# Optimization experiments

Measured on AMD Instinct MI355X. Metric: run time of the kernel, lower is better.

Reference implementation:

```python
import jax, jax.numpy as jnp
import numpy as np

B, S, H = 2, 1024, 4096
NH, NKV, HD = 32, 8, 128
GROUPS = NH // NKV  # 4


def _dequant_linear(x, w_q, scale, bias=None):
    # torch Linear layout: W [out, in]; per-output-channel symmetric dequant
    w = w_q.astype(jnp.float32) * scale[:, None]
    y = jnp.einsum('bsi,oi->bso', x, w)
    if bias is not None:
        y = y + bias
    return y


def setup_inputs() -> dict:
    key = jax.random.key(0)
    ks = jax.random.split(key, 12)
    hidden_states = jax.random.normal(ks[0], (B, S, H), dtype=jnp.float32)
    # additive causal mask: 0 on/below diagonal, large negative above
    causal = jnp.where(jnp.tril(jnp.ones((S, S), dtype=bool)), 0.0, -1e9).astype(jnp.float32)
    attention_mask = jnp.broadcast_to(causal[None, None], (B, 1, S, S))
    # int8-valued quantized weights, per-out-channel scales (~unit-variance effective weight rows / sqrt(fan_in))
    def qw(k, out, inp):
        return jax.random.randint(k, (out, inp), -127, 128, dtype=jnp.int32)
    def sc(k, out):
        return jax.random.uniform(k, (out,), dtype=jnp.float32, minval=1e-4, maxval=3e-4)
    wq_q = qw(ks[1], H, H);            wq_s = sc(ks[2], H)
    wk_q = qw(ks[3], NKV * HD, H);     wk_s = sc(ks[4], NKV * HD)
    wv_q = qw(ks[5], NKV * HD, H);     wv_s = sc(ks[6], NKV * HD)
    wo_q = qw(ks[7], H, H);            wo_s = sc(ks[8], H)
    bq = jax.random.normal(ks[9], (H,), dtype=jnp.float32) * 0.02
    bk = jax.random.normal(ks[10], (NKV * HD,), dtype=jnp.float32) * 0.02
    return {
        'hidden_states': hidden_states, 'attention_mask': attention_mask,
        'wq_q': wq_q, 'wq_s': wq_s, 'bq': bq,
        'wk_q': wk_q, 'wk_s': wk_s, 'bk': bk,
        'wv_q': wv_q, 'wv_s': wv_s,
        'wo_q': wo_q, 'wo_s': wo_s,
    }


def reference(hidden_states, attention_mask, wq_q, wq_s, bq, wk_q, wk_s, bk, wv_q, wv_s, wo_q, wo_s):
    bsz, q_len, _ = hidden_states.shape
    q = _dequant_linear(hidden_states, wq_q, wq_s, bq)      # [B,S,H]
    k = _dequant_linear(hidden_states, wk_q, wk_s, bk)      # [B,S,NKV*HD]
    v = _dequant_linear(hidden_states, wv_q, wv_s)          # [B,S,NKV*HD]
    q = q.reshape(bsz, q_len, NH, HD).transpose(0, 2, 1, 3)     # [B,NH,S,HD]
    k = k.reshape(bsz, q_len, NKV, HD).transpose(0, 2, 1, 3)    # [B,NKV,S,HD]
    v = v.reshape(bsz, q_len, NKV, HD).transpose(0, 2, 1, 3)
    # GQA: repeat_interleave kv heads along head dim
    k = jnp.repeat(k, GROUPS, axis=1)   # [B,NH,S,HD]
    v = jnp.repeat(v, GROUPS, axis=1)
    scores = jnp.einsum('bhqd,bhkd->bhqk', q, k) / np.float32(np.sqrt(HD))
    scores = scores + attention_mask
    attn = jax.nn.softmax(scores.astype(jnp.float32), axis=-1).astype(q.dtype)
    out = jnp.einsum('bhqk,bhkd->bhqd', attn, v)            # [B,NH,S,HD]
    out = out.transpose(0, 2, 1, 3).reshape(bsz, q_len, H)
    out = _dequant_linear(out, wo_q, wo_s)
    return out
```

## Files before the change

### kernel.cpp

```cpp
#include <hip/hip_runtime.h>
#include <math.h>

#define BB   2
#define SS   1024
#define HH   4096
#define NHH  32
#define NKVV 8
#define HDD  128
#define MR   2048
#define KVD  1024
#define NQKVD 6144
#define KD   4096
#define KHALF 2048
#define SCALE_F 0.08838834764831845f

typedef __attribute__((ext_vector_type(8))) short bf16x8;
typedef __attribute__((ext_vector_type(4))) float f32x4;
typedef __attribute__((ext_vector_type(4))) int i32x4;

#define MFMA(a, b, c) __builtin_amdgcn_mfma_f32_16x16x32_bf16((a), (b), (c), 0, 0, 0)
#define MFMA_I8(a, b, c) __builtin_amdgcn_mfma_i32_16x16x64_i8((a), (b), (c), 0, 0, 0)

__device__ __forceinline__ unsigned short f2bf(float f) {
  union { float f; unsigned u; } v; v.f = f;
  return (unsigned short)((v.u + 0x7fffu + ((v.u >> 16) & 1u)) >> 16);
}
__device__ __forceinline__ unsigned short f2h(float f) {
  union { _Float16 h; unsigned short s; } v; v.h = (_Float16)f; return v.s;
}
__device__ __forceinline__ float h2f(unsigned short s) {
  union { unsigned short s; _Float16 h; } v; v.s = s; return (float)v.h;
}
__device__ __forceinline__ float bf2f(unsigned short s) {
  union { unsigned u; float f; } v; v.u = ((unsigned)s) << 16; return v.f;
}
__device__ __forceinline__ float4 ld4h(const unsigned short* p) {
  uint2 d = *(const uint2*)p;
  float4 r;
  r.x = h2f((unsigned short)(d.x & 0xffff)); r.y = h2f((unsigned short)(d.x >> 16));
  r.z = h2f((unsigned short)(d.y & 0xffff)); r.w = h2f((unsigned short)(d.y >> 16));
  return r;
}

__device__ __forceinline__ void gload_lds16(const void* g, void* l) {
  __builtin_amdgcn_global_load_lds(
      (const __attribute__((address_space(1))) void*)g,
      (__attribute__((address_space(3))) void*)l, 16, 0, 0);
}

__device__ __forceinline__ signed char q8(float x, float inv) {
  float r = rintf(x * inv);
  r = fmaxf(-127.f, fminf(127.f, r));
  return (signed char)(int)r;
}

__global__ void cvt_w_i8(const int* __restrict__ in, signed char* __restrict__ out, int n16) {
  int i = blockIdx.x * 256 + threadIdx.x;
  if (i >= n16) return;
  const int4* p = (const int4*)in + (size_t)i * 4;
  union { signed char c[16]; int4 q; } o;
#pragma unroll
  for (int j = 0; j < 4; ++j) {
    int4 v = p[j];
    o.c[j * 4 + 0] = (signed char)v.x; o.c[j * 4 + 1] = (signed char)v.y;
    o.c[j * 4 + 2] = (signed char)v.z; o.c[j * 4 + 3] = (signed char)v.w;
  }
  ((int4*)out)[i] = o.q;
}

__global__ void quant_f32(const float* __restrict__ in, signed char* __restrict__ out,
                          float* __restrict__ scale) {
  __shared__ float wm[4];
  const int row = blockIdx.x;
  const int t = threadIdx.x;
  const float4* p = (const float4*)(in + (size_t)row * HH) + t * 4;
  float4 v[4];
  float m = 0.f;
#pragma unroll
  for (int j = 0; j < 4; ++j) {
    v[j] = p[j];
    m = fmaxf(m, fmaxf(fmaxf(fabsf(v[j].x), fabsf(v[j].y)), fmaxf(fabsf(v[j].z), fabsf(v[j].w))));
  }
#pragma unroll
  for (int o = 32; o; o >>= 1) m = fmaxf(m, __shfl_xor(m, o));
  if ((t & 63) == 0) wm[t >> 6] = m;
  __syncthreads();
  m = fmaxf(fmaxf(wm[0], wm[1]), fmaxf(wm[2], wm[3]));
  m = fmaxf(m, 1e-12f);
  const float inv = 127.f / m;
  union { signed char c[16]; int4 q; } o;
#pragma unroll
  for (int j = 0; j < 4; ++j) {
    o.c[j * 4 + 0] = q8(v[j].x, inv); o.c[j * 4 + 1] = q8(v[j].y, inv);
    o.c[j * 4 + 2] = q8(v[j].z, inv); o.c[j * 4 + 3] = q8(v[j].w, inv);
  }
  ((int4*)(out + (size_t)row * HH))[t] = o.q;
  if (t == 0) scale[row] = m / 127.f;
}

__global__ void quant_bf16(const unsigned short* __restrict__ in, signed char* __restrict__ out,
                           float* __restrict__ scale) {
  __shared__ float wm[4];
  const int row = blockIdx.x;
  const int t = threadIdx.x;
  const uint4* p = (const uint4*)(in + (size_t)row * HH) + t * 2;
  float f[16];
  float m = 0.f;
#pragma unroll
  for (int j = 0; j < 2; ++j) {
    uint4 d = p[j];
    unsigned u[4] = {d.x, d.y, d.z, d.w};
#pragma unroll
    for (int k = 0; k < 4; ++k) {
      f[j * 8 + k * 2] = bf2f((unsigned short)(u[k] & 0xffff));
      f[j * 8 + k * 2 + 1] = bf2f((unsigned short)(u[k] >> 16));
    }
  }
#pragma unroll
  for (int e = 0; e < 16; ++e) m = fmaxf(m, fabsf(f[e]));
#pragma unroll
  for (int o = 32; o; o >>= 1) m = fmaxf(m, __shfl_xor(m, o));
  if ((t & 63) == 0) wm[t >> 6] = m;
  __syncthreads();
  m = fmaxf(fmaxf(wm[0], wm[1]), fmaxf(wm[2], wm[3]));
  m = fmaxf(m, 1e-12f);
  const float inv = 127.f / m;
  union { signed char c[16]; int4 q; } o;
#pragma unroll
  for (int e = 0; e < 16; ++e) o.c[e] = q8(f[e], inv);
  ((int4*)(out + (size_t)row * HH))[t] = o.q;
  if (t == 0) scale[row] = m / 127.f;
}

template <int MODE>
__global__ __launch_bounds__(256) void gemm_i8(
    const signed char* __restrict__ A, const signed char* __restrict__ W,
    const float* __restrict__ sRow,
    const float* __restrict__ s0, const float* __restrict__ s1, const float* __restrict__ s2,
    unsigned short* __restrict__ P, int N) {
  __shared__ signed char ldsA[128 * 64];
  __shared__ signed char ldsB[128 * 64];
  const int t = threadIdx.x;
  const int lane = t & 63;
  const int w = t >> 6;
  const int wr = w & 1, wc = w >> 1;
  const int l15 = lane & 15, quad = lane >> 4;
  const int bm = blockIdx.y, bn = blockIdx.x, kz = blockIdx.z;

  const int srow_ = t >> 2;
  const int scol_ = (t & 3) * 16;
  const signed char* gA = A + (size_t)(bm * 128 + srow_) * KD + scol_ + kz * KHALF;
  const signed char* gW = W + (size_t)(bn * 128 + srow_) * KD + scol_ + kz * KHALF;
  signed char* lA = ldsA + t * 16;
  signed char* lB = ldsB + t * 16;

  i32x4 acc[4][4] = {};

  for (int k0 = 0; k0 < KHALF; k0 += 64) {
    __syncthreads();
    gload_lds16(gA + k0, lA);
    gload_lds16(gA + (size_t)64 * KD + k0, lA + 4096);
    gload_lds16(gW + k0, lB);
    gload_lds16(gW + (size_t)64 * KD + k0, lB + 4096);
    __syncthreads();
    i32x4 af[4], bfr[4];
#pragma unroll
    for (int mi = 0; mi < 4; ++mi)
      af[mi] = *(const i32x4*)(ldsA + (wr * 64 + mi * 16 + l15) * 64 + quad * 16);
#pragma unroll
    for (int ni = 0; ni < 4; ++ni)
      bfr[ni] = *(const i32x4*)(ldsB + (wc * 64 + ni * 16 + l15) * 64 + quad * 16);
#pragma unroll
    for (int mi = 0; mi < 4; ++mi)
#pragma unroll
      for (int ni = 0; ni < 4; ++ni)
        acc[mi][ni] = MFMA_I8(af[mi], bfr[ni], acc[mi][ni]);
  }

  unsigned short* Pz = P + (size_t)kz * MR * N;
  const int row0 = bm * 128 + wr * 64 + quad * 4;
  const int col0 = bn * 128 + wc * 64 + l15;
#pragma unroll
  for (int ni = 0; ni < 4; ++ni) {
    const int col = col0 + ni * 16;
    float sc;
    if (MODE == 0)
      sc = (col < HH) ? s0[col] : (col < HH + KVD) ? s1[col - HH] : s2[col - HH - KVD];
    else
      sc = s0[col];
#pragma unroll
    for (int mi = 0; mi < 4; ++mi)
#pragma unroll
      for (int r = 0; r < 4; ++r) {
        const int row = row0 + mi * 16 + r;
        const float v = (float)acc[mi][ni][r] * sRow[row] * sc;
        Pz[(size_t)row * N + col] = f2h(v);
      }
  }
}

__global__ void epi_qk(const unsigned short* __restrict__ P0, const unsigned short* __restrict__ P1,
                       const float* __restrict__ bQ, const float* __restrict__ bK,
                       unsigned short* __restrict__ oQ, unsigned short* __restrict__ oK) {
  const int col = (blockIdx.x * 256 + threadIdx.x) * 4;
  const int row = blockIdx.y;
  const size_t off = (size_t)row * NQKVD + col;
  float4 a = ld4h(P0 + off), b2 = ld4h(P1 + off);
  union { unsigned short s[4]; uint2 d; } o;
  if (col < HH) {
    const float4 b = *(const float4*)(bQ + col);
    o.s[0] = f2bf(a.x + b2.x + b.x); o.s[1] = f2bf(a.y + b2.y + b.y);
    o.s[2] = f2bf(a.z + b2.z + b.z); o.s[3] = f2bf(a.w + b2.w + b.w);
    *(uint2*)(oQ + (size_t)row * HH + col) = o.d;
  } else {
    const int c = col - HH;
    const float4 b = *(const float4*)(bK + c);
    o.s[0] = f2bf(a.x + b2.x + b.x); o.s[1] = f2bf(a.y + b2.y + b.y);
    o.s[2] = f2bf(a.z + b2.z + b.z); o.s[3] = f2bf(a.w + b2.w + b.w);
    *(uint2*)(oK + (size_t)row * KVD + c) = o.d;
  }
}

__global__ void epi_v(const unsigned short* __restrict__ P0, const unsigned short* __restrict__ P1,
                      unsigned short* __restrict__ oVt) {
  __shared__ unsigned short lds_t[64][65];
  const int t = threadIdx.x;
  const int c0 = blockIdx.x * 64;
  const int r0 = blockIdx.y * 64;
  const int c4 = (t & 15) * 4;
#pragma unroll
  for (int rr = 0; rr < 4; ++rr) {
    const int rl = (t >> 4) * 4 + rr;
    const size_t off = (size_t)(r0 + rl) * NQKVD + (HH + KVD) + c0 + c4;
    float4 a = ld4h(P0 + off), b = ld4h(P1 + off);
    lds_t[c4 + 0][rl] = f2bf(a.x + b.x);
    lds_t[c4 + 1][rl] = f2bf(a.y + b.y);
    lds_t[c4 + 2][rl] = f2bf(a.z + b.z);
    lds_t[c4 + 3][rl] = f2bf(a.w + b.w);
  }
  __syncthreads();
  const int cl = t >> 2;
  const int rs = (t & 3) * 16;
  union { unsigned short s[16]; uint4 q[2]; } o;
#pragma unroll
  for (int i = 0; i < 16; ++i) o.s[i] = lds_t[cl][rs + i];
  uint4* dst = (uint4*)(oVt + (size_t)(c0 + cl) * MR + r0 + rs);
  dst[0] = o.q[0]; dst[1] = o.q[1];
}

__global__ void epi_o(const unsigned short* __restrict__ P0, const unsigned short* __restrict__ P1,
                      float* __restrict__ out) {
  const int col = (blockIdx.x * 256 + threadIdx.x) * 4;
  const int row = blockIdx.y;
  const size_t off = (size_t)row * HH + col;
  float4 a = ld4h(P0 + off), b = ld4h(P1 + off);
  *(float4*)(out + off) = make_float4(a.x + b.x, a.y + b.y, a.z + b.z, a.w + b.w);
}

__global__ __launch_bounds__(256, 3) void attn_kernel(
    const unsigned short* __restrict__ Q,
    const unsigned short* __restrict__ K,
    const unsigned short* __restrict__ Vt,
    unsigned short* __restrict__ O) {
  __shared__ unsigned short ldsK[4 * 64 * 32];
  __shared__ unsigned short ldsV[2 * 128 * 32];
  __shared__ unsigned short ldsP[4][16 * 88];
  const int t = threadIdx.x;
  const int lane = t & 63;
  const int wv = t >> 6;
  const int l15 = lane & 15, quad = lane >> 4;
  const int qt = 15 - blockIdx.x;
  const int h = blockIdx.y;
  const int b = blockIdx.z;
  const int kv = h >> 2;
  const int q0w = qt * 64 + wv * 16;
  const int q = q0w + l15;

  bf16x8 bq[4];
  const unsigned short* qbase = Q + (size_t)(b * SS + q0w + l15) * HH + h * HDD + quad * 8;
#pragma unroll
  for (int kk = 0; kk < 4; ++kk) bq[kk] = *(const bf16x8*)(qbase + kk * 32);

  const unsigned short* gK = K + (size_t)(b * SS) * KVD + kv * HDD + wv * 32 + (lane & 3) * 8;
  const unsigned short* gV = Vt + (size_t)(kv * HDD + wv * 32 + (lane >> 2)) * MR + b * SS + (lane & 3) * 8;
  unsigned short* lK = ldsK + wv * 2048 + lane * 8;
  unsigned short* lV = ldsV + (size_t)wv * 32 * 32 + lane * 8;
  unsigned short* lp = ldsP[wv];

  f32x4 accO[8] = {};
  float m_run = -1e30f, l_run = 0.f;

  for (int kt = 0; kt <= qt; ++kt) {
    const int k0 = kt * 64;
    __syncthreads();
#pragma unroll
    for (int j = 0; j < 4; ++j)
      gload_lds16(gK + (size_t)(k0 + j * 16 + (lane >> 2)) * KVD, lK + j * 512);
#pragma unroll
    for (int kc = 0; kc < 2; ++kc)
#pragma unroll
      for (int j = 0; j < 2; ++j)
        gload_lds16(gV + (size_t)j * 16 * MR + k0 + kc * 32,
                    lV + kc * 4096 + j * 512);
    __syncthreads();

    f32x4 st[4] = {};
#pragma unroll
    for (int kk = 0; kk < 4; ++kk)
#pragma unroll
      for (int mf = 0; mf < 4; ++mf) {
        bf16x8 af = *(const bf16x8*)(ldsK + kk * 2048 + (mf * 16 + l15) * 32 + quad * 8);
        st[mf] = MFMA(af, bq[kk], st[mf]);
      }

    float p[4][4];
    float cm = -1e30f;
#pragma unroll
    for (int mf = 0; mf < 4; ++mf)
#pragma unroll
      for (int r = 0; r < 4; ++r) {
        const int k = k0 + mf * 16 + quad * 4 + r;
        float v = st[mf][r] * SCALE_F;
        if (k > q) v = -1e30f;
        p[mf][r] = v;
        cm = fmaxf(cm, v);
      }
    cm = fmaxf(cm, __shfl_xor(cm, 16));
    cm = fmaxf(cm, __shfl_xor(cm, 32));
    const float mn = fmaxf(m_run, cm);
    const float al = __expf(m_run - mn);
    float sum = 0.f;
#pragma unroll
    for (int mf = 0; mf < 4; ++mf)
#pragma unroll
      for (int r = 0; r < 4; ++r) {
        const float e = __expf(p[mf][r] - mn);
        p[mf][r] = e;
        sum += e;
      }
    sum += __shfl_xor(sum, 16);
    sum += __shfl_xor(sum, 32);
    l_run = l_run * al + sum;
    m_run = mn;
    float af4[4];
#pragma unroll
    for (int r = 0; r < 4; ++r) af4[r] = __shfl(al, quad * 4 + r);
#pragma unroll
    for (int cb = 0; cb < 8; ++cb)
#pragma unroll
      for (int r = 0; r < 4; ++r) accO[cb][r] *= af4[r];

#pragma unroll
    for (int mf = 0; mf < 4; ++mf) {
      union { unsigned short s[4]; unsigned long long d; } pk;
#pragma unroll
      for (int r = 0; r < 4; ++r) pk.s[r] = f2bf(p[mf][r]);
      *(unsigned long long*)(lp + l15 * 88 + mf * 16 + quad * 4) = pk.d;
    }
    bf16x8 ap0 = *(const bf16x8*)(lp + l15 * 88 + quad * 8);
    bf16x8 ap1 = *(const bf16x8*)(lp + l15 * 88 + 32 + quad * 8);

#pragma unroll
    for (int cb = 0; cb < 8; ++cb) {
      bf16x8 bv0 = *(const bf16x8*)(ldsV + (cb * 16 + l15) * 32 + quad * 8);
      bf16x8 bv1 = *(const bf16x8*)(ldsV + 4096 + (cb * 16 + l15) * 32 + quad * 8);
      accO[cb] = MFMA(ap0, bv0, accO[cb]);
      accO[cb] = MFMA(ap1, bv1, accO[cb]);
    }
  }

  float lr[4];
#pragma unroll
  for (int r = 0; r < 4; ++r) lr[r] = __shfl(l_run, quad * 4 + r);
  unsigned short* ob = O + (size_t)(b * SS + q0w + quad * 4) * HH + h * HDD + l15;
#pragma unroll
  for (int cb = 0; cb < 8; ++cb)
#pragma unroll
    for (int r = 0; r < 4; ++r)
      ob[(size_t)r * HH + cb * 16] = f2bf(accO[cb][r] / lr[r]);
}

extern "C" void kernel_launch(void* const* d_in, const int* in_sizes, int n_in,
                              void* d_out, int out_size, void* d_ws, size_t ws_size,
                              hipStream_t stream) {
  const float* x = (const float*)d_in[0];
  const int* wq = (const int*)d_in[2];
  const float* wqs = (const float*)d_in[3];
  const float* bq = (const float*)d_in[4];
  const int* wk = (const int*)d_in[5];
  const float* wks = (const float*)d_in[6];
  const float* bk = (const float*)d_in[7];
  const int* wv = (const int*)d_in[8];
  const float* wvs = (const float*)d_in[9];
  const int* wo = (const int*)d_in[10];
  const float* wos = (const float*)d_in[11];
  float* out = (float*)d_out;
  char* ws = (char*)d_ws;

  signed char*    x_i8    = (signed char*)   (ws + (0ull   << 20));
  signed char*    wqkv_i8 = (signed char*)   (ws + (8ull   << 20));
  signed char*    wo_i8   = (signed char*)   (ws + (32ull  << 20));
  unsigned short* Pq      = (unsigned short*)(ws + (48ull  << 20));
  unsigned short* q_bf    = (unsigned short*)(ws + (0ull   << 20));
  unsigned short* k_bf    = (unsigned short*)(ws + (16ull  << 20));
  unsigned short* v_t     = (unsigned short*)(ws + (20ull  << 20));
  unsigned short* a_bf    = (unsigned short*)(ws + (48ull  << 20));
  signed char*    a_i8    = (signed char*)   (ws + (64ull  << 20));
  unsigned short* Po      = (unsigned short*)(ws + (96ull  << 20));
  float*          sx      = (float*)         (ws + (128ull << 20));
  float*          sa      = (float*)         (ws + (129ull << 20));
  if (ws_size < (130ull << 20)) return;

  quant_f32<<<MR, 256, 0, stream>>>(x, x_i8, sx);
  cvt_w_i8<<<4096, 256, 0, stream>>>(wq, wqkv_i8, HH * HH / 16);
  cvt_w_i8<<<1024, 256, 0, stream>>>(wk, wqkv_i8 + (size_t)HH * HH, KVD * HH / 16);
  cvt_w_i8<<<1024, 256, 0, stream>>>(wv, wqkv_i8 + (size_t)(HH + KVD) * HH, KVD * HH / 16);
  cvt_w_i8<<<4096, 256, 0, stream>>>(wo, wo_i8, HH * HH / 16);

  gemm_i8<0><<<dim3(NQKVD / 128, MR / 128, 2), 256, 0, stream>>>(
      x_i8, wqkv_i8, sx, wqs, wks, wvs, Pq, NQKVD);

  epi_qk<<<dim3(5, MR), 256, 0, stream>>>(Pq, Pq + (size_t)MR * NQKVD, bq, bk, q_bf, k_bf);
  epi_v<<<dim3(16, 32), 256, 0, stream>>>(Pq, Pq + (size_t)MR * NQKVD, v_t);

  attn_kernel<<<dim3(16, NHH, BB), 256, 0, stream>>>(q_bf, k_bf, v_t, a_bf);

  quant_bf16<<<MR, 256, 0, stream>>>(a_bf, a_i8, sa);
  gemm_i8<1><<<dim3(HH / 128, MR / 128, 2), 256, 0, stream>>>(
      a_i8, wo_i8, sa, wos, nullptr, nullptr, Po, HH);
  epi_o<<<dim3(4, MR), 256, 0, stream>>>(Po, Po + (size_t)MR * HH, out);
}
```

Baseline: 454.6 us.

## Merge weight conversion and QKV epilogue launches, deepen GEMM K tile with swizzled LDS

The four weight conversion launches become one kernel, and the Q/K and V epilogues merge into one launch. The int8 GEMM now stages a K chunk of 128 instead of 64 per barrier, with an XOR-swizzled LDS layout meant to avoid bank conflicts. The softmax scale moves out of the attention inner loop and is folded into Q during the epilogue. These aim to cut launch overhead, halve GEMM synchronisations and remove a multiply per score, at the cost of doubled LDS per GEMM block and a slightly different rounding order for Q.

New measurement: 426.5 us. 1.07x faster.

```diff
diff --git a/kernel.cpp b/kernel.cpp
--- a/kernel.cpp
+++ b/kernel.cpp
@@ -54,10 +54,19 @@
   return (signed char)(int)r;
 }
 
-__global__ void cvt_w_i8(const int* __restrict__ in, signed char* __restrict__ out, int n16) {
-  int i = blockIdx.x * 256 + threadIdx.x;
-  if (i >= n16) return;
-  const int4* p = (const int4*)in + (size_t)i * 4;
+#define NQ16 ((size_t)HH * HH / 16)
+#define NK16 ((size_t)KVD * HH / 16)
+__global__ void cvt_w_all(const int* __restrict__ wq, const int* __restrict__ wk,
+                          const int* __restrict__ wv, const int* __restrict__ wo,
+                          signed char* __restrict__ wqkv, signed char* __restrict__ wo8) {
+  size_t i = (size_t)blockIdx.x * 256 + threadIdx.x;
+  const int* src;
+  signed char* dst;
+  if (i < NQ16) { src = wq; dst = wqkv; }
+  else if (i < NQ16 + NK16) { src = wk - NQ16 * 16; dst = wqkv; }
+  else if (i < NQ16 + 2 * NK16) { src = wv - (NQ16 + NK16) * 16; dst = wqkv; }
+  else { src = wo - (NQ16 + 2 * NK16) * 16; dst = wo8 - (NQ16 + 2 * NK16) * 16; }
+  const int4* p = (const int4*)(src + i * 16);
   union { signed char c[16]; int4 q; } o;
 #pragma unroll
   for (int j = 0; j < 4; ++j) {
@@ -65,7 +74,7 @@
     o.c[j * 4 + 0] = (signed char)v.x; o.c[j * 4 + 1] = (signed char)v.y;
     o.c[j * 4 + 2] = (signed char)v.z; o.c[j * 4 + 3] = (signed char)v.w;
   }
-  ((int4*)out)[i] = o.q;
+  *(int4*)(dst + i * 16) = o.q;
 }
 
 __global__ void quant_f32(const float* __restrict__ in, signed char* __restrict__ out,
@@ -138,8 +147,8 @@
     const float* __restrict__ sRow,
     const float* __restrict__ s0, const float* __restrict__ s1, const float* __restrict__ s2,
     unsigned short* __restrict__ P, int N) {
-  __shared__ signed char ldsA[128 * 64];
-  __shared__ signed char ldsB[128 * 64];
+  __shared__ signed char ldsA[128 * 128];
+  __shared__ signed char ldsB[128 * 128];
   const int t = threadIdx.x;
   const int lane = t & 63;
   const int w = t >> 6;
@@ -147,8 +156,8 @@
   const int l15 = lane & 15, quad = lane >> 4;
   const int bm = blockIdx.y, bn = blockIdx.x, kz = blockIdx.z;
 
-  const int srow_ = t >> 2;
-  const int scol_ = (t & 3) * 16;
+  const int srow_ = t >> 3;
+  const int scol_ = ((t & 7) ^ (srow_ & 7)) * 16;
   const signed char* gA = A + (size_t)(bm * 128 + srow_) * KD + scol_ + kz * KHALF;
   const signed char* gW = W + (size_t)(bn * 128 + srow_) * KD + scol_ + kz * KHALF;
   signed char* lA = ldsA + t * 16;
@@ -156,25 +165,35 @@
 
   i32x4 acc[4][4] = {};
 
-  for (int k0 = 0; k0 < KHALF; k0 += 64) {
+  for (int k0 = 0; k0 < KHALF; k0 += 128) {
     __syncthreads();
-    gload_lds16(gA + k0, lA);
-    gload_lds16(gA + (size_t)64 * KD + k0, lA + 4096);
-    gload_lds16(gW + k0, lB);
-    gload_lds16(gW + (size_t)64 * KD + k0, lB + 4096);
+#pragma unroll
+    for (int j = 0; j < 4; ++j) {
+      gload_lds16(gA + (size_t)j * 32 * KD + k0, lA + j * 4096);
+      gload_lds16(gW + (size_t)j * 32 * KD + k0, lB + j * 4096);
+    }
     __syncthreads();
-    i32x4 af[4], bfr[4];
-#pragma unroll
-    for (int mi = 0; mi < 4; ++mi)
-      af[mi] = *(const i32x4*)(ldsA + (wr * 64 + mi * 16 + l15) * 64 + quad * 16);
-#pragma unroll
-    for (int ni = 0; ni < 4; ++ni)
-      bfr[ni] = *(const i32x4*)(ldsB + (wc * 64 + ni * 16 + l15) * 64 + quad * 16);
-#pragma unroll
-    for (int mi = 0; mi < 4; ++mi)
-#pragma unroll
-      for (int ni = 0; ni < 4; ++ni)
-        acc[mi][ni] = MFMA_I8(af[mi], bfr[ni], acc[mi][ni]);
+#pragma unroll
+    for (int kc = 0; kc < 2; ++kc) {
+      i32x4 af[4], bfr[4];
+#pragma unroll
+      for (int mi = 0; mi < 4; ++mi) {
+        const int row = wr * 64 + mi * 16 + l15;
+        const int ch = (kc * 4 + quad) ^ (row & 7);
+        af[mi] = *(const i32x4*)(ldsA + row * 128 + ch * 16);
+      }
+#pragma unroll
+      for (int ni = 0; ni < 4; ++ni) {
+        const int row = wc * 64 + ni * 16 + l15;
+        const int ch = (kc * 4 + quad) ^ (row & 7);
+        bfr[ni] = *(const i32x4*)(ldsB + row * 128 + ch * 16);
+      }
+#pragma unroll
+      for (int mi = 0; mi < 4; ++mi)
+#pragma unroll
+        for (int ni = 0; ni < 4; ++ni)
+          acc[mi][ni] = MFMA_I8(af[mi], bfr[ni], acc[mi][ni]);
+    }
   }
 
   unsigned short* Pz = P + (size_t)kz * MR * N;
@@ -199,53 +218,57 @@
   }
 }
 
-__global__ void epi_qk(const unsigned short* __restrict__ P0, const unsigned short* __restrict__ P1,
-                       const float* __restrict__ bQ, const float* __restrict__ bK,
-                       unsigned short* __restrict__ oQ, unsigned short* __restrict__ oK) {
-  const int col = (blockIdx.x * 256 + threadIdx.x) * 4;
-  const int row = blockIdx.y;
-  const size_t off = (size_t)row * NQKVD + col;
-  float4 a = ld4h(P0 + off), b2 = ld4h(P1 + off);
-  union { unsigned short s[4]; uint2 d; } o;
-  if (col < HH) {
-    const float4 b = *(const float4*)(bQ + col);
-    o.s[0] = f2bf(a.x + b2.x + b.x); o.s[1] = f2bf(a.y + b2.y + b.y);
-    o.s[2] = f2bf(a.z + b2.z + b.z); o.s[3] = f2bf(a.w + b2.w + b.w);
-    *(uint2*)(oQ + (size_t)row * HH + col) = o.d;
-  } else {
-    const int c = col - HH;
-    const float4 b = *(const float4*)(bK + c);
-    o.s[0] = f2bf(a.x + b2.x + b.x); o.s[1] = f2bf(a.y + b2.y + b.y);
-    o.s[2] = f2bf(a.z + b2.z + b.z); o.s[3] = f2bf(a.w + b2.w + b.w);
-    *(uint2*)(oK + (size_t)row * KVD + c) = o.d;
-  }
-}
-
-__global__ void epi_v(const unsigned short* __restrict__ P0, const unsigned short* __restrict__ P1,
-                      unsigned short* __restrict__ oVt) {
+__global__ void epi_qkv(const unsigned short* __restrict__ P0, const unsigned short* __restrict__ P1,
+                        const float* __restrict__ bQ, const float* __restrict__ bK,
+                        unsigned short* __restrict__ oQ, unsigned short* __restrict__ oK,
+                        unsigned short* __restrict__ oVt) {
   __shared__ unsigned short lds_t[64][65];
   const int t = threadIdx.x;
-  const int c0 = blockIdx.x * 64;
-  const int r0 = blockIdx.y * 64;
-  const int c4 = (t & 15) * 4;
-#pragma unroll
-  for (int rr = 0; rr < 4; ++rr) {
-    const int rl = (t >> 4) * 4 + rr;
-    const size_t off = (size_t)(r0 + rl) * NQKVD + (HH + KVD) + c0 + c4;
-    float4 a = ld4h(P0 + off), b = ld4h(P1 + off);
-    lds_t[c4 + 0][rl] = f2bf(a.x + b.x);
-    lds_t[c4 + 1][rl] = f2bf(a.y + b.y);
-    lds_t[c4 + 2][rl] = f2bf(a.z + b.z);
-    lds_t[c4 + 3][rl] = f2bf(a.w + b.w);
-  }
-  __syncthreads();
-  const int cl = t >> 2;
-  const int rs = (t & 3) * 16;
-  union { unsigned short s[16]; uint4 q[2]; } o;
-#pragma unroll
-  for (int i = 0; i < 16; ++i) o.s[i] = lds_t[cl][rs + i];
-  uint4* dst = (uint4*)(oVt + (size_t)(c0 + cl) * MR + r0 + rs);
-  dst[0] = o.q[0]; dst[1] = o.q[1];
+  int bid = blockIdx.x;
+  if (bid < 10240) {
+    const int row = bid / 5;
+    const int col = (bid - row * 5) * 1024 + t * 4;
+    const size_t off = (size_t)row * NQKVD + col;
+    float4 a = ld4h(P0 + off), b2 = ld4h(P1 + off);
+    union { unsigned short s[4]; uint2 d; } o;
+    if (col < HH) {
+      const float4 b = *(const float4*)(bQ + col);
+      o.s[0] = f2bf((a.x + b2.x + b.x) * SCALE_F);
+      o.s[1] = f2bf((a.y + b2.y + b.y) * SCALE_F);
+      o.s[2] = f2bf((a.z + b2.z + b.z) * SCALE_F);
+      o.s[3] = f2bf((a.w + b2.w + b.w) * SCALE_F);
+      *(uint2*)(oQ + (size_t)row * HH + col) = o.d;
+    } else {
+      const int c = col - HH;
+      const float4 b = *(const float4*)(bK + c);
+      o.s[0] = f2bf(a.x + b2.x + b.x); o.s[1] = f2bf(a.y + b2.y + b.y);
+      o.s[2] = f2bf(a.z + b2.z + b.z); o.s[3] = f2bf(a.w + b2.w + b.w);
+      *(uint2*)(oK + (size_t)row * KVD + c) = o.d;
+    }
+  } else {
+    bid -= 10240;
+    const int c0 = (bid & 15) * 64;
+    const int r0 = (bid >> 4) * 64;
+    const int c4 = (t & 15) * 4;
+#pragma unroll
+    for (int rr = 0; rr < 4; ++rr) {
+      const int rl = (t >> 4) * 4 + rr;
+      const size_t off = (size_t)(r0 + rl) * NQKVD + (HH + KVD) + c0 + c4;
+      float4 a = ld4h(P0 + off), b = ld4h(P1 + off);
+      lds_t[c4 + 0][rl] = f2bf(a.x + b.x);
+      lds_t[c4 + 1][rl] = f2bf(a.y + b.y);
+      lds_t[c4 + 2][rl] = f2bf(a.z + b.z);
+      lds_t[c4 + 3][rl] = f2bf(a.w + b.w);
+    }
+    __syncthreads();
+    const int cl = t >> 2;
+    const int rs = (t & 3) * 16;
+    union { unsigned short s[16]; uint4 q[2]; } o;
+#pragma unroll
+    for (int i = 0; i < 16; ++i) o.s[i] = lds_t[cl][rs + i];
+    uint4* dst = (uint4*)(oVt + (size_t)(c0 + cl) * MR + r0 + rs);
+    dst[0] = o.q[0]; dst[1] = o.q[1];
+  }
 }
 
 __global__ void epi_o(const unsigned short* __restrict__ P0, const unsigned short* __restrict__ P1,
@@ -320,7 +343,7 @@
 #pragma unroll
       for (int r = 0; r < 4; ++r) {
         const int k = k0 + mf * 16 + quad * 4 + r;
-        float v = st[mf][r] * SCALE_F;
+        float v = st[mf][r];
         if (k > q) v = -1e30f;
         p[mf][r] = v;
         cm = fmaxf(cm, v);
@@ -412,16 +435,12 @@
   if (ws_size < (130ull << 20)) return;
 
   quant_f32<<<MR, 256, 0, stream>>>(x, x_i8, sx);
-  cvt_w_i8<<<4096, 256, 0, stream>>>(wq, wqkv_i8, HH * HH / 16);
-  cvt_w_i8<<<1024, 256, 0, stream>>>(wk, wqkv_i8 + (size_t)HH * HH, KVD * HH / 16);
-  cvt_w_i8<<<1024, 256, 0, stream>>>(wv, wqkv_i8 + (size_t)(HH + KVD) * HH, KVD * HH / 16);
-  cvt_w_i8<<<4096, 256, 0, stream>>>(wo, wo_i8, HH * HH / 16);
+  cvt_w_all<<<10240, 256, 0, stream>>>(wq, wk, wv, wo, wqkv_i8, wo_i8);
 
   gemm_i8<0><<<dim3(NQKVD / 128, MR / 128, 2), 256, 0, stream>>>(
       x_i8, wqkv_i8, sx, wqs, wks, wvs, Pq, NQKVD);
 
-  epi_qk<<<dim3(5, MR), 256, 0, stream>>>(Pq, Pq + (size_t)MR * NQKVD, bq, bk, q_bf, k_bf);
-  epi_v<<<dim3(16, 32), 256, 0, stream>>>(Pq, Pq + (size_t)MR * NQKVD, v_t);
+  epi_qkv<<<10752, 256, 0, stream>>>(Pq, Pq + (size_t)MR * NQKVD, bq, bk, q_bf, k_bf, v_t);
 
   attn_kernel<<<dim3(16, NHH, BB), 256, 0, stream>>>(q_bf, k_bf, v_t, a_bf);
 
```
